# Kernel tuning notes

Measured on AMD Instinct MI355X. Metric: run time of the kernel, lower is better.

The kernel has to match this reference:

```python
import jax, jax.numpy as jnp
import numpy as np

N_QUBITS = 8
N_LAYERS = 2
CDT = jnp.complex64


def _apply_1q(state, U, w):
    # state: [B] + [2]*n complex; U: [B,2,2] complex; acts on wire w (axis w+1)
    s = jnp.moveaxis(state, w + 1, -1)
    s = jnp.einsum('b...i,bji->b...j', s, U)
    return jnp.moveaxis(s, -1, w + 1)


def _rx(theta):
    t = theta * 0.5
    c, s = jnp.cos(t).astype(CDT), jnp.sin(t).astype(CDT)
    return jnp.stack([jnp.stack([c, -1j * s], -1), jnp.stack([-1j * s, c], -1)], -2)


def _ry(theta):
    t = theta * 0.5
    c, s = jnp.cos(t).astype(CDT), jnp.sin(t).astype(CDT)
    return jnp.stack([jnp.stack([c, -s], -1), jnp.stack([s, c], -1)], -2)


def _rz(theta):
    e = jnp.exp(-0.5j * theta.astype(CDT))
    z = jnp.zeros_like(e)
    return jnp.stack([jnp.stack([e, z], -1), jnp.stack([z, jnp.conj(e)], -1)], -2)


def _cnot(state, c, t):
    # control wire c, target wire t (c < t in this circuit) -> axes c+1, t+1
    s0 = jnp.take(state, jnp.array([0]), axis=c + 1)
    s1 = jnp.take(state, jnp.array([1]), axis=c + 1)
    s1 = jnp.flip(s1, axis=t + 1)
    return jnp.concatenate([s0, s1], axis=c + 1)


def _circuit(x, params):
    n, L = N_QUBITS, N_LAYERS
    B = x.shape[0]
    state = jnp.zeros((B,) + (2,) * n, CDT).at[(slice(None),) + (0,) * n].set(1.0)
    # data encoding: RY(x_i * pi), per-sample angles
    for i in range(n):
        state = _apply_1q(state, _ry(x[:, i] * jnp.pi), i)
    n_rot, n_ent = 3 * n, n * (n - 1) // 2
    for l in range(L):
        base = l * (n_rot + n_ent)
        rot = params[base:base + n_rot]
        ent = params[base + n_rot:base + n_rot + n_ent]
        for i in range(n):
            state = _apply_1q(state, _rx(jnp.broadcast_to(rot[3 * i], (B,))), i)
            state = _apply_1q(state, _ry(jnp.broadcast_to(rot[3 * i + 1], (B,))), i)
            state = _apply_1q(state, _rz(jnp.broadcast_to(rot[3 * i + 2], (B,))), i)
        k = 0
        for i in range(n):
            for j in range(i + 1, n):
                state = _cnot(state, i, j)
                state = _apply_1q(state, _rz(jnp.broadcast_to(ent[k], (B,))), j)
                k += 1
    probs = state.real ** 2 + state.imag ** 2  # [B] + [2]*n
    ev = []
    for w in range(n):
        p = jnp.moveaxis(probs, w + 1, 1).reshape(B, 2, -1).sum(-1)
        ev.append(p[:, 0] - p[:, 1])  # <Z_w>
    return jnp.stack(ev, -1)  # [B, n_qubits]


def setup_inputs() -> dict:
    key = jax.random.key(0)
    k1, k2, k3, k4 = jax.random.split(key, 4)
    B, n, C = 4096, N_QUBITS, 10
    x = jax.random.uniform(k1, (B, n), dtype=jnp.float32)
    params = jax.random.normal(k2, (104,), dtype=jnp.float32) * 0.1
    W = jax.random.normal(k3, (C, n), dtype=jnp.float32) * (1.0 / np.sqrt(n))
    b = jax.random.normal(k4, (C,), dtype=jnp.float32) * 0.01
    return {"x": x, "params": params, "W": W, "b": b}


def reference(x, params, W, b):
    quantum_out = _circuit(x, params)          # [B, n_qubits]
    return quantum_out @ W.T + b               # Linear post-process, [B, n_classes]
```

## Files before the change

kernel.cpp:

```cpp
#include <hip/hip_runtime.h>


#define PI_HALF 1.57079632679489662f

__device__ __forceinline__ float shfx(float v, int m)      { return __shfl_xor(v, m, 64); }
__device__ __forceinline__ float shfl_from(float v, int l) { return __shfl(v, l, 64); }

__global__ __launch_bounds__(640) void vqc_pre(
    const float* __restrict__ prm, float* __restrict__ ws)
{
    const int t = threadIdx.x;
    if (t < 512) {
        const int l = t >> 8, a = t & 255;
        float phi = 0.f;
        int k = 0;
        #pragma unroll
        for (int i = 0; i < 8; ++i)
            #pragma unroll
            for (int j = i + 1; j < 8; ++j, ++k) {
                float th = prm[l * 52 + 24 + k];
                int bit = ((a >> (7 - i)) ^ (a >> (7 - j))) & 1;
                phi += bit ? 0.5f * th : -0.5f * th;
            }
        float c, s;
        __sincosf(phi, &s, &c);
        ws[64 + (l * 256 + a) * 2 + 0] = c;
        ws[64 + (l * 256 + a) * 2 + 1] = s;
    } else if (t < 528) {
        const int idx = t - 512;
        const int l = idx >> 3, q = idx & 7;
        float cx, sx, cy, sy, cz, sz;
        __sincosf(prm[l * 52 + 3 * q    ] * 0.5f, &sx, &cx);
        __sincosf(prm[l * 52 + 3 * q + 1] * 0.5f, &sy, &cy);
        __sincosf(prm[l * 52 + 3 * q + 2] * 0.5f, &sz, &cz);
        float n00r =  cy * cx, n00i =  sy * sx;
        float n01r = -sy * cx, n01i = -cy * sx;
        ws[l * 32 + q * 4 + 0] = cz * n00r + sz * n00i;
        ws[l * 32 + q * 4 + 1] = cz * n00i - sz * n00r;
        ws[l * 32 + q * 4 + 2] = cz * n01r + sz * n01i;
        ws[l * 32 + q * 4 + 3] = cz * n01i - sz * n01r;
    }
}

__global__ __launch_bounds__(256) void vqc_main(
    const float* __restrict__ x,
    const float* __restrict__ ws,
    const float* __restrict__ W,
    const float* __restrict__ bvec,
    float* __restrict__ out)
{
    const int lane = threadIdx.x & 63;
    const int bi = __builtin_amdgcn_readfirstlane((blockIdx.x << 2) + (threadIdx.x >> 6));

    float cw[8], swv[8];
    #pragma unroll
    for (int w = 0; w < 8; ++w) {
        float ang = x[bi * 8 + w] * PI_HALF;
        __sincosf(ang, &swv[w], &cw[w]);
    }
    float base = 1.f;
    #pragma unroll
    for (int w = 0; w < 6; ++w)
        base *= ((lane >> (5 - w)) & 1) ? swv[w] : cw[w];
    float re[4], im[4];
    re[0] = base * cw[6]  * cw[7];  re[1] = base * cw[6]  * swv[7];
    re[2] = base * swv[6] * cw[7];  re[3] = base * swv[6] * swv[7];
    im[0] = im[1] = im[2] = im[3] = 0.f;

    const int pr = __popc(lane) & 1;
    int g = lane; g ^= g >> 1; g ^= g >> 2; g ^= g >> 4;
    const int src_lane = g;

    #pragma unroll
    for (int l = 0; l < 2; ++l) {
        #pragma unroll
        for (int i = 0; i < 8; ++i) {
            const float ar  = ws[l * 32 + i * 4 + 0];
            const float ai  = ws[l * 32 + i * 4 + 1];
            const float br  = ws[l * 32 + i * 4 + 2];
            const float bi_ = ws[l * 32 + i * 4 + 3];
            const int p = 7 - i;
            if (p >= 2) {
                const int mk = 1 << (p - 2);
                const int h  = (lane >> (p - 2)) & 1;
                const float Ai = h ? -ai : ai;
                const float Br = h ? -br : br;
                #pragma unroll
                for (int r = 0; r < 4; ++r) {
                    float pre = shfx(re[r], mk), pim = shfx(im[r], mk);
                    float cr = re[r], ci = im[r];
                    re[r] = ar * cr - Ai * ci + Br * pre - bi_ * pim;
                    im[r] = ar * ci + Ai * cr + Br * pim + bi_ * pre;
                }
            } else if (p == 1) {
                #pragma unroll
                for (int r0i = 0; r0i < 2; ++r0i) {
                    const int i0 = r0i, i1 = r0i + 2;
                    float r0 = re[i0], i0v = im[i0], r1 = re[i1], i1v = im[i1];
                    re[i0] =  ar * r0 - ai * i0v + br * r1 - bi_ * i1v;
                    im[i0] =  ar * i0v + ai * r0 + br * i1v + bi_ * r1;
                    re[i1] = -br * r0 - bi_ * i0v + ar * r1 + ai * i1v;
                    im[i1] = -br * i0v + bi_ * r0 + ar * i1v - ai * r1;
                }
            } else {
                #pragma unroll
                for (int r0i = 0; r0i < 2; ++r0i) {
                    const int i0 = 2 * r0i, i1 = 2 * r0i + 1;
                    float r0 = re[i0], i0v = im[i0], r1 = re[i1], i1v = im[i1];
                    re[i0] =  ar * r0 - ai * i0v + br * r1 - bi_ * i1v;
                    im[i0] =  ar * i0v + ai * r0 + br * i1v + bi_ * r1;
                    re[i1] = -br * r0 - bi_ * i0v + ar * r1 + ai * i1v;
                    im[i1] = -br * i0v + bi_ * r0 + ar * i1v - ai * r1;
                }
            }
        }

        const float4* ph = (const float4*)(ws + 64 + l * 512);
        float4 f0 = ph[lane * 2], f1 = ph[lane * 2 + 1];
        {
            float nr, ni;
            nr = f0.x * re[0] - f0.y * im[0]; ni = f0.x * im[0] + f0.y * re[0]; re[0] = nr; im[0] = ni;
            nr = f0.z * re[1] - f0.w * im[1]; ni = f0.z * im[1] + f0.w * re[1]; re[1] = nr; im[1] = ni;
            nr = f1.x * re[2] - f1.y * im[2]; ni = f1.x * im[2] + f1.y * re[2]; re[2] = nr; im[2] = ni;
            nr = f1.z * re[3] - f1.w * im[3]; ni = f1.z * im[3] + f1.w * re[3]; re[3] = nr; im[3] = ni;
        }

        float Bre[4], Bim[4];
        #pragma unroll
        for (int m = 0; m < 4; ++m) {
            Bre[m] = shfl_from(re[m], src_lane);
            Bim[m] = shfl_from(im[m], src_lane);
        }
        re[0] = pr ? Bre[3] : Bre[0];  im[0] = pr ? Bim[3] : Bim[0];
        re[1] = pr ? Bre[2] : Bre[1];  im[1] = pr ? Bim[2] : Bim[1];
        re[2] = pr ? Bre[0] : Bre[3];  im[2] = pr ? Bim[0] : Bim[3];
        re[3] = pr ? Bre[1] : Bre[2];  im[3] = pr ? Bim[1] : Bim[2];
    }

    float p0 = re[0]*re[0] + im[0]*im[0];
    float p1 = re[1]*re[1] + im[1]*im[1];
    float p2 = re[2]*re[2] + im[2]*im[2];
    float p3 = re[3]*re[3] + im[3]*im[3];
    float psum = p0 + p1 + p2 + p3;

    float v = psum;
    #pragma unroll
    for (int m = 1; m < 64; m <<= 1) {
        float pp = shfx(v, m);
        v = (lane & m) ? (pp - v) : (v + pp);
    }
    float q6 = p0 + p1 - p2 - p3;
    float q7 = p0 - p1 + p2 - p3;
    #pragma unroll
    for (int m = 1; m < 64; m <<= 1) { q6 += shfx(q6, m); q7 += shfx(q7, m); }

    float e0 = shfl_from(v, 32), e1 = shfl_from(v, 16), e2 = shfl_from(v, 8);
    float e3 = shfl_from(v, 4),  e4 = shfl_from(v, 2),  e5 = shfl_from(v, 1);

    if (lane < 10) {
        const float* Wr = W + lane * 8;
        float acc = bvec[lane];
        acc += e0 * Wr[0] + e1 * Wr[1] + e2 * Wr[2] + e3 * Wr[3];
        acc += e4 * Wr[4] + e5 * Wr[5] + q6 * Wr[6] + q7 * Wr[7];
        out[bi * 10 + lane] = acc;
    }
}

extern "C" void kernel_launch(void* const* d_in, const int* in_sizes, int n_in,
                              void* d_out, int out_size, void* d_ws, size_t ws_size,
                              hipStream_t stream) {
    const float* x    = (const float*)d_in[0];
    const float* prm  = (const float*)d_in[1];
    const float* W    = (const float*)d_in[2];
    const float* bvec = (const float*)d_in[3];
    float* out = (float*)d_out;
    float* ws  = (float*)d_ws;

    vqc_pre<<<1, 640, 0, stream>>>(prm, ws);

    const int B = in_sizes[0] / 8;
    vqc_main<<<B / 4, 256, 0, stream>>>(x, ws, W, bvec, out);
}
```

Baseline: 17.64 us.

## Fuse parameter precompute into main kernel and skip final CNOT permutation shuffle

Removes the separate single-block precompute kernel and its workspace round-trip. Each wave now computes the fused rotation coefficients in lanes and broadcasts them with readlane, and evaluates the entangling-phase angles inline with sign-flip tricks. The second-layer CNOT permutation is dropped by remapping which lanes and sign patterns the expectation values are read from. This saves one kernel launch and a dependency, at the cost of redundant transcendental work in every wave.

```diff
diff --git a/kernel.cpp b/kernel.cpp
--- a/kernel.cpp
+++ b/kernel.cpp
@@ -5,46 +5,16 @@
 
 __device__ __forceinline__ float shfx(float v, int m)      { return __shfl_xor(v, m, 64); }
 __device__ __forceinline__ float shfl_from(float v, int l) { return __shfl(v, l, 64); }
-
-__global__ __launch_bounds__(640) void vqc_pre(
-    const float* __restrict__ prm, float* __restrict__ ws)
-{
-    const int t = threadIdx.x;
-    if (t < 512) {
-        const int l = t >> 8, a = t & 255;
-        float phi = 0.f;
-        int k = 0;
-        #pragma unroll
-        for (int i = 0; i < 8; ++i)
-            #pragma unroll
-            for (int j = i + 1; j < 8; ++j, ++k) {
-                float th = prm[l * 52 + 24 + k];
-                int bit = ((a >> (7 - i)) ^ (a >> (7 - j))) & 1;
-                phi += bit ? 0.5f * th : -0.5f * th;
-            }
-        float c, s;
-        __sincosf(phi, &s, &c);
-        ws[64 + (l * 256 + a) * 2 + 0] = c;
-        ws[64 + (l * 256 + a) * 2 + 1] = s;
-    } else if (t < 528) {
-        const int idx = t - 512;
-        const int l = idx >> 3, q = idx & 7;
-        float cx, sx, cy, sy, cz, sz;
-        __sincosf(prm[l * 52 + 3 * q    ] * 0.5f, &sx, &cx);
-        __sincosf(prm[l * 52 + 3 * q + 1] * 0.5f, &sy, &cy);
-        __sincosf(prm[l * 52 + 3 * q + 2] * 0.5f, &sz, &cz);
-        float n00r =  cy * cx, n00i =  sy * sx;
-        float n01r = -sy * cx, n01i = -cy * sx;
-        ws[l * 32 + q * 4 + 0] = cz * n00r + sz * n00i;
-        ws[l * 32 + q * 4 + 1] = cz * n00i - sz * n00r;
-        ws[l * 32 + q * 4 + 2] = cz * n01r + sz * n01i;
-        ws[l * 32 + q * 4 + 3] = cz * n01i - sz * n01r;
-    }
-}
-
-__global__ __launch_bounds__(256) void vqc_main(
+__device__ __forceinline__ float rdlane(float v, int l) {
+    return __int_as_float(__builtin_amdgcn_readlane(__float_as_int(v), l));
+}
+__device__ __forceinline__ float sgnterm(float th, int pword) {
+    return __int_as_float(__float_as_int(-th) ^ (int)((unsigned)pword << 31));
+}
+
+__global__ __launch_bounds__(256) void vqc_fused(
     const float* __restrict__ x,
-    const float* __restrict__ ws,
+    const float* __restrict__ prm,
     const float* __restrict__ W,
     const float* __restrict__ bvec,
     float* __restrict__ out)
@@ -52,11 +22,31 @@
     const int lane = threadIdx.x & 63;
     const int bi = __builtin_amdgcn_readfirstlane((blockIdx.x << 2) + (threadIdx.x >> 6));
 
+    float mar, mai, mbr, mbi;
+    {
+        const int t = lane & 15;
+        const int l = t >> 3, q = t & 7;
+        const float* p3 = prm + l * 52 + 3 * q;
+        float cx, sx, cy, sy, cz, sz;
+        __sincosf(p3[0] * 0.5f, &sx, &cx);
+        __sincosf(p3[1] * 0.5f, &sy, &cy);
+        __sincosf(p3[2] * 0.5f, &sz, &cz);
+        float n00r =  cy * cx, n00i =  sy * sx;
+        float n01r = -sy * cx, n01i = -cy * sx;
+        mar = cz * n00r + sz * n00i;
+        mai = cz * n00i - sz * n00r;
+        mbr = cz * n01r + sz * n01i;
+        mbi = cz * n01i - sz * n01r;
+    }
+
     float cw[8], swv[8];
-    #pragma unroll
-    for (int w = 0; w < 8; ++w) {
-        float ang = x[bi * 8 + w] * PI_HALF;
-        __sincosf(ang, &swv[w], &cw[w]);
+    {
+        const float4 x0 = ((const float4*)(x + bi * 8))[0];
+        const float4 x1 = ((const float4*)(x + bi * 8))[1];
+        float xv[8] = {x0.x, x0.y, x0.z, x0.w, x1.x, x1.y, x1.z, x1.w};
+        #pragma unroll
+        for (int w = 0; w < 8; ++w)
+            __sincosf(xv[w] * PI_HALF, &swv[w], &cw[w]);
     }
     float base = 1.f;
     #pragma unroll
@@ -67,6 +57,10 @@
     re[2] = base * swv[6] * cw[7];  re[3] = base * swv[6] * swv[7];
     im[0] = im[1] = im[2] = im[3] = 0.f;
 
+    int lb[6];
+    #pragma unroll
+    for (int b = 0; b < 6; ++b) lb[b] = lane >> b;
+
     const int pr = __popc(lane) & 1;
     int g = lane; g ^= g >> 1; g ^= g >> 2; g ^= g >> 4;
     const int src_lane = g;
@@ -75,10 +69,11 @@
     for (int l = 0; l < 2; ++l) {
         #pragma unroll
         for (int i = 0; i < 8; ++i) {
-            const float ar  = ws[l * 32 + i * 4 + 0];
-            const float ai  = ws[l * 32 + i * 4 + 1];
-            const float br  = ws[l * 32 + i * 4 + 2];
-            const float bi_ = ws[l * 32 + i * 4 + 3];
+            const int srcl = l * 8 + i;
+            const float ar  = rdlane(mar, srcl);
+            const float ai  = rdlane(mai, srcl);
+            const float br  = rdlane(mbr, srcl);
+            const float bi_ = rdlane(mbi, srcl);
             const int p = 7 - i;
             if (p >= 2) {
                 const int mk = 1 << (p - 2);
@@ -115,26 +110,47 @@
             }
         }
 
-        const float4* ph = (const float4*)(ws + 64 + l * 512);
-        float4 f0 = ph[lane * 2], f1 = ph[lane * 2 + 1];
         {
-            float nr, ni;
-            nr = f0.x * re[0] - f0.y * im[0]; ni = f0.x * im[0] + f0.y * re[0]; re[0] = nr; im[0] = ni;
-            nr = f0.z * re[1] - f0.w * im[1]; ni = f0.z * im[1] + f0.w * re[1]; re[1] = nr; im[1] = ni;
-            nr = f1.x * re[2] - f1.y * im[2]; ni = f1.x * im[2] + f1.y * re[2]; re[2] = nr; im[2] = ni;
-            nr = f1.z * re[3] - f1.w * im[3]; ni = f1.z * im[3] + f1.w * re[3]; re[3] = nr; im[3] = ni;
+            const float* pb = prm + l * 52 + 24;
+            float A = 0.f, B6 = 0.f, B7 = 0.f, T = 0.f;
+            int k = 0;
+            #pragma unroll
+            for (int i = 0; i < 8; ++i) {
+                #pragma unroll
+                for (int j = i + 1; j < 8; ++j, ++k) {
+                    const float th = pb[k];
+                    if (j <= 5)      A  += sgnterm(th, lb[5 - i] ^ lb[5 - j]);
+                    else if (i == 6) T   = th;
+                    else if (j == 6) B6 += sgnterm(th, lb[5 - i]);
+                    else             B7 += sgnterm(th, lb[5 - i]);
+                }
+            }
+            const float AB  = A + B6, AmB = A - B6;
+            const float BmT = B7 - T, BpT = B7 + T;
+            float ph[4] = { 0.5f * (AB  + BmT), 0.5f * (AB  - BmT),
+                            0.5f * (AmB + BpT), 0.5f * (AmB - BpT) };
+            #pragma unroll
+            for (int r = 0; r < 4; ++r) {
+                float c, s;
+                __sincosf(ph[r], &s, &c);
+                float nr = c * re[r] - s * im[r];
+                float ni = c * im[r] + s * re[r];
+                re[r] = nr; im[r] = ni;
+            }
         }
 
-        float Bre[4], Bim[4];
-        #pragma unroll
-        for (int m = 0; m < 4; ++m) {
-            Bre[m] = shfl_from(re[m], src_lane);
-            Bim[m] = shfl_from(im[m], src_lane);
+        if (l == 0) {
+            float Bre[4], Bim[4];
+            #pragma unroll
+            for (int m = 0; m < 4; ++m) {
+                Bre[m] = shfl_from(re[m], src_lane);
+                Bim[m] = shfl_from(im[m], src_lane);
+            }
+            re[0] = pr ? Bre[3] : Bre[0];  im[0] = pr ? Bim[3] : Bim[0];
+            re[1] = pr ? Bre[2] : Bre[1];  im[1] = pr ? Bim[2] : Bim[1];
+            re[2] = pr ? Bre[0] : Bre[3];  im[2] = pr ? Bim[0] : Bim[3];
+            re[3] = pr ? Bre[1] : Bre[2];  im[3] = pr ? Bim[1] : Bim[2];
         }
-        re[0] = pr ? Bre[3] : Bre[0];  im[0] = pr ? Bim[3] : Bim[0];
-        re[1] = pr ? Bre[2] : Bre[1];  im[1] = pr ? Bim[2] : Bim[1];
-        re[2] = pr ? Bre[0] : Bre[3];  im[2] = pr ? Bim[0] : Bim[3];
-        re[3] = pr ? Bre[1] : Bre[2];  im[3] = pr ? Bim[1] : Bim[2];
     }
 
     float p0 = re[0]*re[0] + im[0]*im[0];
@@ -149,19 +165,23 @@
         float pp = shfx(v, m);
         v = (lane & m) ? (pp - v) : (v + pp);
     }
-    float q6 = p0 + p1 - p2 - p3;
-    float q7 = p0 - p1 + p2 - p3;
-    #pragma unroll
-    for (int m = 1; m < 64; m <<= 1) { q6 += shfx(q6, m); q7 += shfx(q7, m); }
-
-    float e0 = shfl_from(v, 32), e1 = shfl_from(v, 16), e2 = shfl_from(v, 8);
-    float e3 = shfl_from(v, 4),  e4 = shfl_from(v, 2),  e5 = shfl_from(v, 1);
+    float t6 = p0 + p1 - p2 - p3;  t6 = (lane & 1) ? -t6 : t6;
+    float t7 = p0 - p1 - p2 + p3;
+    #pragma unroll
+    for (int m = 1; m < 64; m <<= 1) { t6 += shfx(t6, m); t7 += shfx(t7, m); }
+
+    const float e0 = shfl_from(v, 32);
+    const float e1 = shfl_from(v, 48);
+    const float e2 = shfl_from(v, 24);
+    const float e3 = shfl_from(v, 12);
+    const float e4 = shfl_from(v, 6);
+    const float e5 = shfl_from(v, 3);
 
     if (lane < 10) {
         const float* Wr = W + lane * 8;
         float acc = bvec[lane];
         acc += e0 * Wr[0] + e1 * Wr[1] + e2 * Wr[2] + e3 * Wr[3];
-        acc += e4 * Wr[4] + e5 * Wr[5] + q6 * Wr[6] + q7 * Wr[7];
+        acc += e4 * Wr[4] + e5 * Wr[5] + t6 * Wr[6] + t7 * Wr[7];
         out[bi * 10 + lane] = acc;
     }
 }
@@ -174,10 +194,7 @@
     const float* W    = (const float*)d_in[2];
     const float* bvec = (const float*)d_in[3];
     float* out = (float*)d_out;
-    float* ws  = (float*)d_ws;
-
-    vqc_pre<<<1, 640, 0, stream>>>(prm, ws);
 
     const int B = in_sizes[0] / 8;
-    vqc_main<<<B / 4, 256, 0, stream>>>(x, ws, W, bvec, out);
-}
+    vqc_fused<<<B / 4, 256, 0, stream>>>(x, prm, W, bvec, out);
+}
```

Measured after the change: 14.19 us. 19.6% less time.
